# Performance work log

Hardware: AMD Instinct MI355X
Metric: run time of the kernel (lower is better)

The kernel has to match this reference:

```python
import jax, jax.numpy as jnp
import numpy as np

NUM_HEADS = 16
ROPE_BASE = 2048.0


def _rope_tables(seq_len, head_dim, dtype):
    inv_freq = 1.0 / (ROPE_BASE ** (jnp.arange(0, head_dim, 2, dtype=jnp.float32) / head_dim))
    t = jnp.arange(seq_len, dtype=jnp.float32)
    freqs = jnp.einsum('i,j->ij', t, inv_freq)          # [N, D/2]
    emb = jnp.concatenate([freqs, freqs], axis=-1)       # [N, D]
    return jnp.cos(emb).astype(dtype), jnp.sin(emb).astype(dtype)


def _rotate_half(x):
    x1, x2 = jnp.split(x, 2, axis=-1)
    return jnp.concatenate([-x2, x1], axis=-1)


def setup_inputs() -> dict:
    key = jax.random.key(0)
    k1, k2, k3, k4 = jax.random.split(key, 4)
    B, N, C = 2, 2048, 1024
    x = jax.random.normal(k1, (B, N, C), dtype=jnp.float32)
    w_qkv = jax.random.normal(k2, (3 * C, C), dtype=jnp.float32) * (C ** -0.5)
    w_proj = jax.random.normal(k3, (C, C), dtype=jnp.float32) * (C ** -0.5)
    b_proj = jnp.zeros((C,), dtype=jnp.float32)
    key_padding_mask = jax.random.randint(k4, (B, N), 0, 2, dtype=jnp.int32)
    return {"x": x, "w_qkv": w_qkv, "w_proj": w_proj, "b_proj": b_proj,
            "key_padding_mask": key_padding_mask}


def reference(x, w_qkv, w_proj, b_proj, key_padding_mask):
    B, N, C = x.shape
    H = NUM_HEADS
    D = C // H
    scale = D ** -0.5

    qkv = x @ w_qkv.T                                    # [B, N, 3C]
    q, k, v = jnp.split(qkv, 3, axis=-1)
    # [B, N, C] -> [B, H, N, D]
    q = q.reshape(B, N, H, D).transpose(0, 2, 1, 3)
    k = k.reshape(B, N, H, D).transpose(0, 2, 1, 3)
    v = v.reshape(B, N, H, D).transpose(0, 2, 1, 3)

    cos, sin = _rope_tables(N, D, x.dtype)               # [N, D]
    q = q * cos + _rotate_half(q) * sin
    k = k * cos + _rotate_half(k) * sin

    attn = jnp.einsum('bhqd,bhkd->bhqk', q, k) * scale   # [B, H, N, N]
    mask = (key_padding_mask == 0)[:, None, None, :]     # [B, 1, 1, N]
    attn = jnp.where(mask, jnp.asarray(-1e9, attn.dtype), attn)
    attn = jax.nn.softmax(attn, axis=-1)

    out = jnp.einsum('bhqk,bhkd->bhqd', attn, v)         # [B, H, N, D]
    out = out.transpose(0, 2, 1, 3).reshape(B, N, C)
    return out @ w_proj.T + b_proj
```

## Files before the change

kernel.cpp:

```cpp
#include <hip/hip_runtime.h>


typedef __attribute__((ext_vector_type(8))) short          s16x8;
typedef __attribute__((ext_vector_type(8))) unsigned short u16x8;
typedef __attribute__((ext_vector_type(4))) unsigned short u16x4;
typedef __attribute__((ext_vector_type(4))) float          f32x4;
typedef __attribute__((ext_vector_type(16))) float         f32x16;
typedef __attribute__((ext_vector_type(4))) unsigned int   u32x4;

#define MFMA_BF16(a, b, c) __builtin_amdgcn_mfma_f32_16x16x32_bf16((a), (b), (c), 0, 0, 0)
#define MFMA32_BF16(a, b, c) __builtin_amdgcn_mfma_f32_32x32x16_bf16((a), (b), (c), 0, 0, 0)

#define GLD_TO_LDS(gp, lp) __builtin_amdgcn_global_load_lds(                  \
    (const __attribute__((address_space(1))) void*)(gp),                      \
    (__attribute__((address_space(3))) void*)(lp), 16, 0, 0)

__device__ __forceinline__ unsigned short f2bf(float f) {
    union { float f; unsigned int u; } v; v.f = f;
    unsigned int u = v.u;
    unsigned int r = u + 0x7FFFu + ((u >> 16) & 1u);
    return (unsigned short)(r >> 16);
}
__device__ __forceinline__ float bf2f(unsigned short h) {
    union { unsigned int u; float f; } v; v.u = ((unsigned int)h) << 16;
    return v.f;
}
__device__ __forceinline__ f32x16 zero16() {
    f32x16 z;
#pragma unroll
    for (int i = 0; i < 16; i++) z[i] = 0.f;
    return z;
}
__device__ __forceinline__ unsigned int pkbf(float a, float b) {
    return __builtin_amdgcn_perm(__builtin_bit_cast(unsigned int, b),
                                 __builtin_bit_cast(unsigned int, a), 0x07060302u);
}
__device__ __forceinline__ int perm16(int p) {
    return (p & 3) + 8 * ((p >> 2) & 1) + 4 * (p >> 3);
}

__global__ __launch_bounds__(256) void prep(const float* __restrict__ x,
                                            const float* __restrict__ wqkv,
                                            const float* __restrict__ wproj,
                                            const int* __restrict__ m,
                                            unsigned short* __restrict__ xb,
                                            unsigned short* __restrict__ wqkvb,
                                            unsigned short* __restrict__ wprojb,
                                            unsigned short* __restrict__ mb) {
    int blk = blockIdx.x, tid = threadIdx.x;
    if (blk < 8192) {
        const float* src; unsigned short* dst; int i;
        if (blk < 4096)      { src = x;     dst = xb;     i = blk * 256 + tid; }
        else if (blk < 7168) { src = wqkv;  dst = wqkvb;  i = (blk - 4096) * 256 + tid; }
        else                 { src = wproj; dst = wprojb; i = (blk - 7168) * 256 + tid; }
        f32x4 v = ((const f32x4*)src)[i];
        u16x4 o;
        o[0] = f2bf(v[0]); o[1] = f2bf(v[1]); o[2] = f2bf(v[2]); o[3] = f2bf(v[3]);
        ((u16x4*)dst)[i] = o;
    } else {
        int i = (blk - 8192) * 256 + tid;
        int src = (i & ~15) | perm16(i & 15);
        mb[i] = (m[src] == 0) ? (unsigned short)0 : (unsigned short)0x3F80;
    }
}

__global__ __launch_bounds__(256) void gemm_bt(const unsigned short* __restrict__ A,
                                               const unsigned short* __restrict__ B,
                                               unsigned short* __restrict__ C,
                                               int M, int N, int K) {
    __shared__ unsigned short Al[128][64];
    __shared__ unsigned short Bl[128][64];
    const int tid  = threadIdx.x;
    const int lane = tid & 63;
    const int qd   = lane >> 4;
    const int cc   = lane & 15;
    const int wave = tid >> 6;
    const int wr   = wave >> 1, wc = wave & 1;
    const int nbx  = N >> 7;
    const int nwg  = gridDim.x;
    int d = blockIdx.x;
    int s = (nwg % 8 == 0) ? (d % 8) * (nwg / 8) + d / 8 : d;
    const int m0   = (s / nbx) * 128, n0 = (s % nbx) * 128;
    unsigned short* Alf = &Al[0][0];
    unsigned short* Blf = &Bl[0][0];

    f32x4 acc[4][4];
#pragma unroll
    for (int i = 0; i < 4; i++)
#pragma unroll
        for (int j = 0; j < 4; j++) acc[i][j] = (f32x4){0.f, 0.f, 0.f, 0.f};

    for (int k0 = 0; k0 < K; k0 += 64) {
#pragma unroll
        for (int t = 0; t < 4; t++) {
            int idx = t * 256 + tid;
            int row = idx >> 3, sg = (idx & 7) ^ (row & 7);
            GLD_TO_LDS(A + (size_t)(m0 + row) * K + k0 + sg * 8, Alf + idx * 8);
            GLD_TO_LDS(B + (size_t)(n0 + row) * K + k0 + sg * 8, Blf + idx * 8);
        }
        __syncthreads();
#pragma unroll
        for (int ks = 0; ks < 64; ks += 32) {
            const int s4 = ks >> 3;
            s16x8 af[4], bf[4];
#pragma unroll
            for (int i = 0; i < 4; i++) {
                int r = wr * 64 + i * 16 + cc;
                af[i] = *(const s16x8*)&Al[r][((s4 + qd) ^ (r & 7)) * 8];
            }
#pragma unroll
            for (int j = 0; j < 4; j++) {
                int r = wc * 64 + j * 16 + cc;
                bf[j] = *(const s16x8*)&Bl[r][((s4 + qd) ^ (r & 7)) * 8];
            }
#pragma unroll
            for (int i = 0; i < 4; i++)
#pragma unroll
                for (int j = 0; j < 4; j++)
                    acc[i][j] = MFMA_BF16(af[i], bf[j], acc[i][j]);
        }
        __syncthreads();
    }
#pragma unroll
    for (int i = 0; i < 4; i++)
#pragma unroll
        for (int j = 0; j < 4; j++)
#pragma unroll
            for (int r = 0; r < 4; r++) {
                int row = m0 + wr * 64 + i * 16 + qd * 4 + r;
                int col = n0 + wc * 64 + j * 16 + cc;
                C[(size_t)row * N + col] = f2bf(acc[i][j][r]);
            }
}

__global__ __launch_bounds__(256) void rope_scatter(const unsigned short* __restrict__ qkv,
                                                    const int* __restrict__ msk,
                                                    unsigned short* __restrict__ Q,
                                                    unsigned short* __restrict__ Kg,
                                                    unsigned short* __restrict__ Vt) {
    const int N = 2048, H = 16, D = 64, C3 = 3072;
    const float SCL = 0.18033688f;
    __shared__ unsigned short vl[64][65];
    const int nt = blockIdx.x, h = blockIdx.y, b = blockIdx.z;
    const int n0 = nt * 64;
    const int tid = threadIdx.x;
    const size_t bh = (size_t)b * H + h;
#pragma unroll
    for (int it = 0; it < 2; it++) {
        int idx = tid + it * 256;
        int row = idx >> 3, seg = idx & 7;
        int d0 = seg * 8;
        int n = n0 + row;
        size_t rb = ((size_t)b * N + n) * C3;
        int keep = msk[(size_t)b * N + n];
        u16x8 qv = *(const u16x8*)&qkv[rb + h * 64 + d0];
        u16x8 qp = *(const u16x8*)&qkv[rb + h * 64 + (d0 ^ 32)];
        u16x8 kv = *(const u16x8*)&qkv[rb + 1024 + h * 64 + d0];
        u16x8 kp = *(const u16x8*)&qkv[rb + 1024 + h * 64 + (d0 ^ 32)];
        u16x8 vv = *(const u16x8*)&qkv[rb + 2048 + h * 64 + d0];
        u16x8 qo, ko;
        float sgn = (d0 < 32) ? -1.0f : 1.0f;
#pragma unroll
        for (int j = 0; j < 8; j++) {
            int jj = (d0 & 31) + j;
            float th = (float)n * exp2f(-0.34375f * (float)jj);
            float cth = cosf(th), sth = sinf(th);
            qo[j] = f2bf((bf2f(qv[j]) * cth + sgn * bf2f(qp[j]) * sth) * SCL);
            ko[j] = f2bf(bf2f(kv[j]) * cth + sgn * bf2f(kp[j]) * sth);
            vl[row][d0 + j] = keep ? vv[j] : (unsigned short)0;
        }
        *(u16x8*)&Q[(bh * N + n) * D + d0]  = qo;
        *(u16x8*)&Kg[(bh * N + n) * D + d0] = ko;
    }
    __syncthreads();
#pragma unroll
    for (int it = 0; it < 2; it++) {
        int idx = tid + it * 256;
        int drow = idx >> 3, nseg = idx & 7;
        u16x8 ov;
#pragma unroll
        for (int j = 0; j < 8; j++) {
            int cpos = nseg * 8 + j;
            int srcl = (cpos & ~15) | perm16(cpos & 15);
            ov[j] = vl[srcl][drow];
        }
        *(u16x8*)&Vt[(bh * D + drow) * N + n0 + nseg * 8] = ov;
    }
}

__global__ __launch_bounds__(256, 1) void flash_attn(const unsigned short* __restrict__ Q,
                                                     const unsigned short* __restrict__ Kg,
                                                     const unsigned short* __restrict__ Vt,
                                                     const unsigned short* __restrict__ mb,
                                                     unsigned short* __restrict__ Og) {
    const int N = 2048, H = 16, D = 64;
    __shared__ unsigned short Kl0[64][64], Kl1[64][64];
    __shared__ unsigned short Vl0[64][64], Vl1[64][64];
    const int tid  = threadIdx.x;
    const int lane = tid & 63;
    const int wave = tid >> 6;
    const int c    = lane & 31;
    const int hi   = lane >> 5;
    int dd = blockIdx.x;
    int sw = (dd & 7) * 32 + (dd >> 3);
    const int qt = sw & 7, h = (sw >> 3) & 15, b = sw >> 7;
    const int q0 = qt * 256;
    const size_t bh = (size_t)b * H + h;

    s16x8 qf[2][4];
#pragma unroll
    for (int qs = 0; qs < 2; qs++) {
        const unsigned short* Qb = Q + (bh * N + q0 + wave * 64 + qs * 32 + c) * D;
#pragma unroll
        for (int kd = 0; kd < 4; kd++) qf[qs][kd] = *(const s16x8*)(Qb + kd * 16 + hi * 8);
    }

    f32x16 o[2][2], lacc[2];
#pragma unroll
    for (int qs = 0; qs < 2; qs++) {
        o[qs][0] = zero16(); o[qs][1] = zero16(); lacc[qs] = zero16();
    }

    const unsigned short* Kbase = Kg + bh * N * D;
    const unsigned short* Vbase = Vt + bh * D * N;
    const unsigned short* mbase = mb + (size_t)b * N;
    const int row_s = tid >> 3, sg_s = (tid & 7) ^ ((tid >> 3) & 7);
    const int row_s2 = (tid + 256) >> 3, sg_s2 = (tid & 7) ^ (((tid + 256) >> 3) & 7);

    auto issue = [&](int k0, unsigned short* Kb, unsigned short* Vb) {
        GLD_TO_LDS(Kbase + (size_t)(k0 + row_s) * D + sg_s * 8,   Kb + tid * 8);
        GLD_TO_LDS(Vbase + (size_t)row_s * N + k0 + sg_s * 8,     Vb + tid * 8);
        GLD_TO_LDS(Kbase + (size_t)(k0 + row_s2) * D + sg_s2 * 8, Kb + (tid + 256) * 8);
        GLD_TO_LDS(Vbase + (size_t)row_s2 * N + k0 + sg_s2 * 8,   Vb + (tid + 256) * 8);
    };

    auto compute = [&](int k0, const unsigned short (*Kb)[64], const unsigned short (*Vb)[64]) {
        auto packkg = [&](const f32x16& sstv, s16x8* pa) {
            float p[16];
#pragma unroll
            for (int r = 0; r < 16; r++) p[r] = __builtin_amdgcn_exp2f(sstv[r]);
#pragma unroll
            for (int half = 0; half < 2; half++) {
                int bs = half * 8;
                u32x4 w = { pkbf(p[bs + 0], p[bs + 1]), pkbf(p[bs + 2], p[bs + 3]),
                            pkbf(p[bs + 4], p[bs + 5]), pkbf(p[bs + 6], p[bs + 7]) };
                pa[half] = __builtin_bit_cast(s16x8, w);
            }
        };

        s16x8 pa[2][4];
#pragma unroll
        for (int kg = 0; kg < 2; kg++) {
            int kr = kg * 32 + c;
            s16x8 kf[4];
#pragma unroll
            for (int kd = 0; kd < 4; kd++)
                kf[kd] = *(const s16x8*)&Kb[kr][((kd * 2 + hi) ^ (kr & 7)) * 8];
            f32x16 sst0 = zero16(), sst1 = zero16();
            __builtin_amdgcn_s_setprio(1);
#pragma unroll
            for (int kd = 0; kd < 4; kd++) {
                sst0 = MFMA32_BF16(kf[kd], qf[0][kd], sst0);
                sst1 = MFMA32_BF16(kf[kd], qf[1][kd], sst1);
            }
            __builtin_amdgcn_s_setprio(0);
            packkg(sst0, &pa[0][kg * 2]);
            packkg(sst1, &pa[1][kg * 2]);
        }

#pragma unroll
        for (int ks = 0; ks < 4; ks++) {
            s16x8 mfr = *(const s16x8*)&mbase[k0 + ks * 16 + hi * 8];
            int vr0 = c, vr1 = 32 + c;
            s16x8 vf0 = *(const s16x8*)&Vb[vr0][((ks * 2 + hi) ^ (vr0 & 7)) * 8];
            s16x8 vf1 = *(const s16x8*)&Vb[vr1][((ks * 2 + hi) ^ (vr1 & 7)) * 8];
            __builtin_amdgcn_s_setprio(1);
#pragma unroll
            for (int qs = 0; qs < 2; qs++) {
                lacc[qs] = MFMA32_BF16(pa[qs][ks], mfr, lacc[qs]);
                o[qs][0] = MFMA32_BF16(pa[qs][ks], vf0, o[qs][0]);
                o[qs][1] = MFMA32_BF16(pa[qs][ks], vf1, o[qs][1]);
            }
            __builtin_amdgcn_s_setprio(0);
        }
    };

    issue(0, &Kl0[0][0], &Vl0[0][0]);
    __syncthreads();
    for (int it = 0; it < 32; it += 2) {
        int k0 = it * 64;
        if (it + 1 < 32) issue(k0 + 64, &Kl1[0][0], &Vl1[0][0]);
        compute(k0, Kl0, Vl0);
        __syncthreads();
        if (it + 2 < 32) issue(k0 + 128, &Kl0[0][0], &Vl0[0][0]);
        compute(k0 + 64, Kl1, Vl1);
        __syncthreads();
    }

#pragma unroll
    for (int qs = 0; qs < 2; qs++) {
        float linv[16];
#pragma unroll
        for (int r = 0; r < 16; r++) linv[r] = 1.0f / lacc[qs][r];
#pragma unroll
        for (int db = 0; db < 2; db++)
#pragma unroll
            for (int r = 0; r < 16; r++) {
                int n = q0 + wave * 64 + qs * 32 + (r & 3) + 8 * (r >> 2) + 4 * hi;
                Og[((size_t)b * N + n) * 1024 + h * 64 + db * 32 + c] =
                    f2bf(o[qs][db][r] * linv[r]);
            }
    }
}

__global__ __launch_bounds__(256) void gemm_proj(const unsigned short* __restrict__ A,
                                                 const unsigned short* __restrict__ B,
                                                 float* __restrict__ C,
                                                 const float* __restrict__ bias) {
    const int NN = 1024, K = 1024;
    __shared__ unsigned short Al[128][64];
    __shared__ unsigned short Bl[64][64];
    const int tid  = threadIdx.x;
    const int lane = tid & 63;
    const int qd   = lane >> 4;
    const int cc   = lane & 15;
    const int wave = tid >> 6;
    const int wr   = wave >> 1, wc = wave & 1;
    int dd = blockIdx.x;
    int sw = (dd & 7) * 64 + (dd >> 3);
    const int m0   = (sw >> 4) * 128, n0 = (sw & 15) * 64;
    unsigned short* Alf = &Al[0][0];
    unsigned short* Blf = &Bl[0][0];

    f32x4 acc[4][2];
#pragma unroll
    for (int i = 0; i < 4; i++)
#pragma unroll
        for (int j = 0; j < 2; j++) acc[i][j] = (f32x4){0.f, 0.f, 0.f, 0.f};

    for (int k0 = 0; k0 < K; k0 += 64) {
#pragma unroll
        for (int t = 0; t < 4; t++) {
            int idx = t * 256 + tid;
            int row = idx >> 3, sg = (idx & 7) ^ (row & 7);
            GLD_TO_LDS(A + (size_t)(m0 + row) * K + k0 + sg * 8, Alf + idx * 8);
        }
#pragma unroll
        for (int t = 0; t < 2; t++) {
            int idx = t * 256 + tid;
            int row = idx >> 3, sg = (idx & 7) ^ (row & 7);
            GLD_TO_LDS(B + (size_t)(n0 + row) * K + k0 + sg * 8, Blf + idx * 8);
        }
        __syncthreads();
#pragma unroll
        for (int ks = 0; ks < 64; ks += 32) {
            const int s4 = ks >> 3;
            s16x8 af[4], bf[2];
#pragma unroll
            for (int i = 0; i < 4; i++) {
                int r = wr * 64 + i * 16 + cc;
                af[i] = *(const s16x8*)&Al[r][((s4 + qd) ^ (r & 7)) * 8];
            }
#pragma unroll
            for (int j = 0; j < 2; j++) {
                int r = wc * 32 + j * 16 + cc;
                bf[j] = *(const s16x8*)&Bl[r][((s4 + qd) ^ (r & 7)) * 8];
            }
#pragma unroll
            for (int i = 0; i < 4; i++)
#pragma unroll
                for (int j = 0; j < 2; j++)
                    acc[i][j] = MFMA_BF16(af[i], bf[j], acc[i][j]);
        }
        __syncthreads();
    }
#pragma unroll
    for (int i = 0; i < 4; i++)
#pragma unroll
        for (int j = 0; j < 2; j++)
#pragma unroll
            for (int r = 0; r < 4; r++) {
                int row = m0 + wr * 64 + i * 16 + qd * 4 + r;
                int col = n0 + wc * 32 + j * 16 + cc;
                C[(size_t)row * NN + col] = acc[i][j][r] + bias[col];
            }
}

extern "C" void kernel_launch(void* const* d_in, const int* in_sizes, int n_in,
                              void* d_out, int out_size, void* d_ws, size_t ws_size,
                              hipStream_t stream) {
    const float* x      = (const float*)d_in[0];
    const float* w_qkv  = (const float*)d_in[1];
    const float* w_proj = (const float*)d_in[2];
    const float* b_proj = (const float*)d_in[3];
    const int*   mask   = (const int*)d_in[4];
    float* out = (float*)d_out;

    unsigned short* ws     = (unsigned short*)d_ws;
    unsigned short* xb     = ws;
    unsigned short* wqkvb  = xb     + (size_t)4096 * 1024;
    unsigned short* wprojb = wqkvb  + (size_t)3072 * 1024;
    unsigned short* qkv    = wprojb + (size_t)1024 * 1024;
    unsigned short* Qm     = qkv    + (size_t)4096 * 3072;
    unsigned short* Km     = Qm     + (size_t)32 * 2048 * 64;
    unsigned short* Vtm    = Km     + (size_t)32 * 2048 * 64;
    unsigned short* attno  = Vtm    + (size_t)32 * 2048 * 64;
    unsigned short* maskbf = attno  + (size_t)4096 * 1024;

    prep<<<8208, 256, 0, stream>>>(x, w_qkv, w_proj, mask, xb, wqkvb, wprojb, maskbf);
    gemm_bt<<<768, 256, 0, stream>>>(xb, wqkvb, qkv, 4096, 3072, 1024);
    rope_scatter<<<dim3(32, 16, 2), 256, 0, stream>>>(qkv, mask, Qm, Km, Vtm);
    flash_attn<<<256, 256, 0, stream>>>(Qm, Km, Vtm, maskbf, attno);
    gemm_proj<<<512, 256, 0, stream>>>(attno, wprojb, out, b_proj);
}
```

Baseline: 187.7 us.

## Split flash attention key tiles across wave pairs and double grid size

Each block now covers 128 query rows instead of 256, and the grid grows from 256 to 512 blocks. Within a block, waves are paired so each wave computes half of every 64-key tile, and the partial O and row sums are reduced through LDS at the end. The goal is more parallelism and occupancy (launch bounds raised to 2 blocks per CU) on a 256-CU device that previously had one block per CU. The cost is an extra LDS reduction with syncs at the end, and each K/V tile is loaded by twice as many blocks overall.

```diff
diff --git a/kernel.cpp b/kernel.cpp
--- a/kernel.cpp
+++ b/kernel.cpp
@@ -188,29 +188,34 @@
     }
 }
 
-__global__ __launch_bounds__(256, 1) void flash_attn(const unsigned short* __restrict__ Q,
+__global__ __launch_bounds__(256, 2) void flash_attn(const unsigned short* __restrict__ Q,
                                                      const unsigned short* __restrict__ Kg,
                                                      const unsigned short* __restrict__ Vt,
                                                      const unsigned short* __restrict__ mb,
                                                      unsigned short* __restrict__ Og) {
     const int N = 2048, H = 16, D = 64;
-    __shared__ unsigned short Kl0[64][64], Kl1[64][64];
-    __shared__ unsigned short Vl0[64][64], Vl1[64][64];
+    __shared__ unsigned short ldsbuf[4 * 64 * 64];
+    unsigned short (*Kl0)[64] = (unsigned short(*)[64])(ldsbuf);
+    unsigned short (*Kl1)[64] = (unsigned short(*)[64])(ldsbuf + 4096);
+    unsigned short (*Vl0)[64] = (unsigned short(*)[64])(ldsbuf + 8192);
+    unsigned short (*Vl1)[64] = (unsigned short(*)[64])(ldsbuf + 12288);
     const int tid  = threadIdx.x;
     const int lane = tid & 63;
     const int wave = tid >> 6;
+    const int qhalf = wave & 1;
+    const int khalf = wave >> 1;
     const int c    = lane & 31;
     const int hi   = lane >> 5;
     int dd = blockIdx.x;
-    int sw = (dd & 7) * 32 + (dd >> 3);
-    const int qt = sw & 7, h = (sw >> 3) & 15, b = sw >> 7;
-    const int q0 = qt * 256;
+    int sw = (dd & 7) * 64 + (dd >> 3);
+    const int qt = sw & 15, h = (sw >> 4) & 15, b = sw >> 8;
+    const int q0 = qt * 128;
     const size_t bh = (size_t)b * H + h;
 
     s16x8 qf[2][4];
 #pragma unroll
     for (int qs = 0; qs < 2; qs++) {
-        const unsigned short* Qb = Q + (bh * N + q0 + wave * 64 + qs * 32 + c) * D;
+        const unsigned short* Qb = Q + (bh * N + q0 + qhalf * 64 + qs * 32 + c) * D;
 #pragma unroll
         for (int kd = 0; kd < 4; kd++) qf[qs][kd] = *(const s16x8*)(Qb + kd * 16 + hi * 8);
     }
@@ -248,28 +253,26 @@
             }
         };
 
-        s16x8 pa[2][4];
-#pragma unroll
-        for (int kg = 0; kg < 2; kg++) {
-            int kr = kg * 32 + c;
-            s16x8 kf[4];
-#pragma unroll
-            for (int kd = 0; kd < 4; kd++)
-                kf[kd] = *(const s16x8*)&Kb[kr][((kd * 2 + hi) ^ (kr & 7)) * 8];
-            f32x16 sst0 = zero16(), sst1 = zero16();
-            __builtin_amdgcn_s_setprio(1);
-#pragma unroll
-            for (int kd = 0; kd < 4; kd++) {
-                sst0 = MFMA32_BF16(kf[kd], qf[0][kd], sst0);
-                sst1 = MFMA32_BF16(kf[kd], qf[1][kd], sst1);
-            }
-            __builtin_amdgcn_s_setprio(0);
-            packkg(sst0, &pa[0][kg * 2]);
-            packkg(sst1, &pa[1][kg * 2]);
-        }
-
-#pragma unroll
-        for (int ks = 0; ks < 4; ks++) {
+        int kr = khalf * 32 + c;
+        s16x8 kf[4];
+#pragma unroll
+        for (int kd = 0; kd < 4; kd++)
+            kf[kd] = *(const s16x8*)&Kb[kr][((kd * 2 + hi) ^ (kr & 7)) * 8];
+        f32x16 sst0 = zero16(), sst1 = zero16();
+        __builtin_amdgcn_s_setprio(1);
+#pragma unroll
+        for (int kd = 0; kd < 4; kd++) {
+            sst0 = MFMA32_BF16(kf[kd], qf[0][kd], sst0);
+            sst1 = MFMA32_BF16(kf[kd], qf[1][kd], sst1);
+        }
+        __builtin_amdgcn_s_setprio(0);
+        s16x8 pa[2][2];
+        packkg(sst0, pa[0]);
+        packkg(sst1, pa[1]);
+
+#pragma unroll
+        for (int ksl = 0; ksl < 2; ksl++) {
+            int ks = khalf * 2 + ksl;
             s16x8 mfr = *(const s16x8*)&mbase[k0 + ks * 16 + hi * 8];
             int vr0 = c, vr1 = 32 + c;
             s16x8 vf0 = *(const s16x8*)&Vb[vr0][((ks * 2 + hi) ^ (vr0 & 7)) * 8];
@@ -277,9 +280,9 @@
             __builtin_amdgcn_s_setprio(1);
 #pragma unroll
             for (int qs = 0; qs < 2; qs++) {
-                lacc[qs] = MFMA32_BF16(pa[qs][ks], mfr, lacc[qs]);
-                o[qs][0] = MFMA32_BF16(pa[qs][ks], vf0, o[qs][0]);
-                o[qs][1] = MFMA32_BF16(pa[qs][ks], vf1, o[qs][1]);
+                lacc[qs]  = MFMA32_BF16(pa[qs][ksl], mfr, lacc[qs]);
+                o[qs][0]  = MFMA32_BF16(pa[qs][ksl], vf0, o[qs][0]);
+                o[qs][1]  = MFMA32_BF16(pa[qs][ksl], vf1, o[qs][1]);
             }
             __builtin_amdgcn_s_setprio(0);
         }
@@ -297,19 +300,42 @@
         __syncthreads();
     }
 
+    float* red = (float*)ldsbuf;
 #pragma unroll
     for (int qs = 0; qs < 2; qs++) {
-        float linv[16];
-#pragma unroll
-        for (int r = 0; r < 16; r++) linv[r] = 1.0f / lacc[qs][r];
-#pragma unroll
-        for (int db = 0; db < 2; db++)
+        __syncthreads();
+        if (khalf == 1) {
+            float* dst = red + qhalf * 3136 + lane * 49;
 #pragma unroll
             for (int r = 0; r < 16; r++) {
-                int n = q0 + wave * 64 + qs * 32 + (r & 3) + 8 * (r >> 2) + 4 * hi;
-                Og[((size_t)b * N + n) * 1024 + h * 64 + db * 32 + c] =
-                    f2bf(o[qs][db][r] * linv[r]);
-            }
+                dst[r] = o[qs][0][r]; dst[16 + r] = o[qs][1][r]; dst[32 + r] = lacc[qs][r];
+            }
+        }
+        __syncthreads();
+        if (khalf == 0) {
+            const float* src = red + qhalf * 3136 + lane * 49;
+#pragma unroll
+            for (int r = 0; r < 16; r++) {
+                o[qs][0][r] += src[r]; o[qs][1][r] += src[16 + r]; lacc[qs][r] += src[32 + r];
+            }
+        }
+    }
+
+    if (khalf == 0) {
+#pragma unroll
+        for (int qs = 0; qs < 2; qs++) {
+            float linv[16];
+#pragma unroll
+            for (int r = 0; r < 16; r++) linv[r] = 1.0f / lacc[qs][r];
+#pragma unroll
+            for (int db = 0; db < 2; db++)
+#pragma unroll
+                for (int r = 0; r < 16; r++) {
+                    int n = q0 + qhalf * 64 + qs * 32 + (r & 3) + 8 * (r >> 2) + 4 * hi;
+                    Og[((size_t)b * N + n) * 1024 + h * 64 + db * 32 + c] =
+                        f2bf(o[qs][db][r] * linv[r]);
+                }
+        }
     }
 }
 
@@ -410,6 +436,6 @@
     prep<<<8208, 256, 0, stream>>>(x, w_qkv, w_proj, mask, xb, wqkvb, wprojb, maskbf);
     gemm_bt<<<768, 256, 0, stream>>>(xb, wqkvb, qkv, 4096, 3072, 1024);
     rope_scatter<<<dim3(32, 16, 2), 256, 0, stream>>>(qkv, mask, Qm, Km, Vtm);
-    flash_attn<<<256, 256, 0, stream>>>(Qm, Km, Vtm, maskbf, attno);
+    flash_attn<<<512, 256, 0, stream>>>(Qm, Km, Vtm, maskbf, attno);
     gemm_proj<<<512, 256, 0, stream>>>(attno, wprojb, out, b_proj);
 }
```

Result: no change. 185.6 us (-1.1%).
